# Performance work log

Measured on AMD Instinct MI355X. Metric: run time of the kernel, lower is better.

## Reference

```python
import jax, jax.numpy as jnp
import numpy as np

IN_FEAT = 512   # input_feature_size
ACT_FEAT = 512  # action_feature_size
HIDDEN = 1024   # output_feature_size
L, B = 128, 64


def setup_inputs() -> dict:
    key = jax.random.key(0)
    ks = jax.random.split(key, 4)
    scale = 1.0 / np.sqrt(HIDDEN)
    return {
        "input_feature": jax.random.normal(ks[0], (B, IN_FEAT), jnp.float32),
        "action_features_data": jax.random.normal(ks[1], (L, B, ACT_FEAT), jnp.float32),
        "hidden_state": jnp.zeros((B, HIDDEN), jnp.float32),
        "state": jnp.zeros((B, HIDDEN), jnp.float32),
        "W_ih": jax.random.normal(ks[2], (4 * HIDDEN, IN_FEAT + ACT_FEAT), jnp.float32) * scale,
        "W_hh": jax.random.normal(ks[3], (4 * HIDDEN, HIDDEN), jnp.float32) * scale,
        "b_ih": jnp.zeros((4 * HIDDEN,), jnp.float32),
        "b_hh": jnp.zeros((4 * HIDDEN,), jnp.float32),
    }


def _lstm_forward(input_feature, acts, h0, c0, W_ih, W_hh, b_ih, b_hh):
    H = h0.shape[-1]
    # Split the input weight into the static (input_feature) and per-step (action) parts.
    W_x = W_ih[:, : input_feature.shape[-1]]   # [4H, in_feat]
    W_a = W_ih[:, input_feature.shape[-1]:]    # [4H, act_feat]
    # Precompute all input-side gate preactivations in one big GEMM: [L, B, 4H]
    pre = jnp.einsum("lba,ga->lbg", acts, W_a) + (input_feature @ W_x.T + b_ih + b_hh)

    def step(carry, pre_t):
        h, c = carry
        gates = pre_t + h @ W_hh.T            # [B, 4H]
        i, f, g, o = jnp.split(gates, 4, axis=-1)  # torch LSTMCell gate order
        i = jax.nn.sigmoid(i)
        f = jax.nn.sigmoid(f)
        g = jnp.tanh(g)
        o = jax.nn.sigmoid(o)
        c1 = f * c + i * g
        h1 = o * jnp.tanh(c1)
        return (h1, c1), h1

    (h_n, c_n), hs = jax.lax.scan(step, (h0, c0), pre)
    return hs, h_n, c_n


def reference(input_feature, action_features_data, hidden_state, state,
              W_ih, W_hh, b_ih, b_hh):
    return _lstm_forward(input_feature, action_features_data, hidden_state, state,
                         W_ih, W_hh, b_ih, b_hh)
```

## Files before the change

### kernel.cpp

```cpp
#include <hip/hip_runtime.h>
#include <hip/hip_bf16.h>

typedef __bf16 bf16x8 __attribute__((ext_vector_type(8)));
typedef float f32x4 __attribute__((ext_vector_type(4)));
typedef unsigned long long ull;

#define HN_OFF 8388608u
#define CN_OFF 8454144u

__device__ __forceinline__ float bf2f(ushort u) {
  union { unsigned int i; float f; } x; x.i = ((unsigned int)u) << 16; return x.f;
}
__device__ __forceinline__ ushort f2bf(float f) {
  union { float f; unsigned int i; } x; x.f = f;
  unsigned int r = x.i + 0x7FFFu + ((x.i >> 16) & 1u);
  return (ushort)(r >> 16);
}

__global__ __launch_bounds__(256) void conv_copy(const float* __restrict__ s,
                                                 ushort* __restrict__ d, int n4) {
  int i = blockIdx.x * 256 + threadIdx.x;
  if (i < n4) {
    float4 v = reinterpret_cast<const float4*>(s)[i];
    ushort4 o; o.x = f2bf(v.x); o.y = f2bf(v.y); o.z = f2bf(v.z); o.w = f2bf(v.w);
    reinterpret_cast<ushort4*>(d)[i] = o;
  }
}

__global__ __launch_bounds__(256) void conv_h0(const float* __restrict__ h0,
                                               ushort* __restrict__ hb) {
  int t = blockIdx.x * 256 + threadIdx.x;
  int b = t >> 7, c = t & 127;
  float4 v0 = *reinterpret_cast<const float4*>(h0 + (size_t)b * 1024 + c * 8);
  float4 v1 = *reinterpret_cast<const float4*>(h0 + (size_t)b * 1024 + c * 8 + 4);
  size_t de = ((size_t)(b >> 4) * 32 + (c >> 2)) * 512 + (size_t)(c & 3) * 128 + (b & 15) * 8;
  ushort* d = hb + de;
  d[0] = f2bf(v0.x); d[1] = f2bf(v0.y); d[2] = f2bf(v0.z); d[3] = f2bf(v0.w);
  d[4] = f2bf(v1.x); d[5] = f2bf(v1.y); d[6] = f2bf(v1.z); d[7] = f2bf(v1.w);
}

__global__ __launch_bounds__(256) void conv_wa(const float* __restrict__ Wih,
                                               ushort* __restrict__ Wa) {
  int t = blockIdx.x * 256 + threadIdx.x;
  int g = t >> 7, c = t & 127;
  float4 v = *reinterpret_cast<const float4*>(Wih + (size_t)g * 1024 + 512 + c * 4);
  ushort4 o; o.x = f2bf(v.x); o.y = f2bf(v.y); o.z = f2bf(v.z); o.w = f2bf(v.w);
  *reinterpret_cast<ushort4*>(Wa + (size_t)g * 512 + c * 4) = o;
}

__global__ __launch_bounds__(256) void base_kernel(const float* __restrict__ x,
    const float* __restrict__ Wih, const float* __restrict__ bih,
    const float* __restrict__ bhh, float* __restrict__ baseT) {
  int t = blockIdx.x * 256 + threadIdx.x;
  int g = t >> 6, b = t & 63;
  const float4* xv = reinterpret_cast<const float4*>(x + (size_t)b * 512);
  const float4* wv = reinterpret_cast<const float4*>(Wih + (size_t)g * 1024);
  float s = 0.f;
  #pragma unroll 4
  for (int a = 0; a < 128; ++a) {
    float4 xa = xv[a], wa = wv[a];
    s += xa.x * wa.x + xa.y * wa.y + xa.z * wa.z + xa.w * wa.w;
  }
  baseT[t] = s + bih[g] + bhh[g];
}

__global__ __launch_bounds__(256, 1) void gemm_pre(
    const ushort* __restrict__ A,
    const ushort* __restrict__ B,
    const float* __restrict__ baseT,
    ushort* __restrict__ C) {
  __shared__ ushort At[128 * 64];
  __shared__ ushort Bt[128 * 64];
  const int tid = threadIdx.x;
  const int m0 = blockIdx.x * 128;
  const int n0 = blockIdx.y * 128;
  const int wave = tid >> 6, lane = tid & 63;
  const int wm = wave >> 1, wn = wave & 1;
  const int q = lane >> 4, lc = lane & 15;

  f32x4 acc[4][4];
  #pragma unroll
  for (int mt = 0; mt < 4; ++mt)
    #pragma unroll
    for (int nt = 0; nt < 4; ++nt)
      acc[mt][nt] = (f32x4){0.f, 0.f, 0.f, 0.f};

  for (int k0 = 0; k0 < 512; k0 += 64) {
    __syncthreads();
    for (int idx = tid; idx < 1024; idx += 256) {
      int r = idx >> 3, ch = idx & 7;
      *reinterpret_cast<uint4*>(&At[r * 64 + (ch ^ (r & 7)) * 8]) =
          *reinterpret_cast<const uint4*>(A + (size_t)(m0 + r) * 512 + k0 + ch * 8);
      *reinterpret_cast<uint4*>(&Bt[r * 64 + (ch ^ (r & 7)) * 8]) =
          *reinterpret_cast<const uint4*>(B + (size_t)(n0 + r) * 512 + k0 + ch * 8);
    }
    __syncthreads();
    #pragma unroll
    for (int kk = 0; kk < 2; ++kk) {
      bf16x8 af[4], bfr[4];
      #pragma unroll
      for (int mt = 0; mt < 4; ++mt) {
        int r = wm * 64 + mt * 16 + lc;
        af[mt] = *reinterpret_cast<const bf16x8*>(&At[r * 64 + ((kk * 4 + q) ^ (r & 7)) * 8]);
      }
      #pragma unroll
      for (int nt = 0; nt < 4; ++nt) {
        int r = wn * 64 + nt * 16 + lc;
        bfr[nt] = *reinterpret_cast<const bf16x8*>(&Bt[r * 64 + ((kk * 4 + q) ^ (r & 7)) * 8]);
      }
      #pragma unroll
      for (int mt = 0; mt < 4; ++mt)
        #pragma unroll
        for (int nt = 0; nt < 4; ++nt)
          acc[mt][nt] = __builtin_amdgcn_mfma_f32_16x16x32_bf16(af[mt], bfr[nt], acc[mt][nt], 0, 0, 0);
    }
  }
  #pragma unroll
  for (int mt = 0; mt < 4; ++mt) {
    #pragma unroll
    for (int nt = 0; nt < 4; ++nt) {
      int g = m0 + wm * 64 + mt * 16 + q * 4;
      int lb = n0 + wn * 64 + nt * 16 + lc;
      int b = lb & 63;
      #pragma unroll
      for (int i = 0; i < 4; ++i) {
        float v = acc[mt][nt][i] + baseT[(size_t)(g + i) * 64 + b];
        C[(size_t)(g + i) * 8192 + lb] = f2bf(v);
      }
    }
  }
}

#define WAITG(n) asm volatile("s_waitcnt vmcnt(" #n ")" ::: "memory"); \
                 __builtin_amdgcn_sched_barrier(0);

__global__ __launch_bounds__(256, 1) void lstm_rec(
    const ushort* __restrict__ Whh,
    const ushort* __restrict__ pre,
    const float* __restrict__ c0,
    const ushort* __restrict__ hbuf,
    ushort* __restrict__ hbw,
    float* __restrict__ out,
    int* __restrict__ flags) {
  __shared__ ushort hstage[16 * 16];
  const int tid = threadIdx.x;
  const int bid = blockIdx.x;
  const int bq = bid & 3;
  const int ug = bid >> 2;
  const int w = tid >> 6;
  const int lane = tid & 63;
  const int q = lane >> 4;
  const int lc = lane & 15;
  const int ul = w * 4 + (lc & 3);
  const int u = ug * 16 + ul;
  const int gr = u + ((lc >> 2) << 10);
  const int bbase = bq * 16 + q * 4;
  const bool cellLane = ((lc & 12) == 0);

  bf16x8 wfr[32];
  {
    const ushort* wr = Whh + (size_t)gr * 1024 + q * 8;
    #pragma unroll
    for (int kk = 0; kk < 32; ++kk)
      wfr[kk] = *reinterpret_cast<const bf16x8*>(wr + kk * 32);
  }

  float cst[4];
  #pragma unroll
  for (int i = 0; i < 4; ++i)
    cst[i] = cellLane ? c0[(size_t)(bbase + i) * 1024 + u] : 0.f;

  const unsigned va_base = ((unsigned)gr * 8192u + (unsigned)bbase) * 2u;
  const unsigned hob0 = ((unsigned)bq << 15) | ((unsigned)lane << 4);

  ushort4 pa = *reinterpret_cast<const ushort4*>(pre + (size_t)gr * 8192 + bbase);

  for (int t = 0; t < 128; ++t) {
    if (t > 0 && w == 0) {
      for (;;) {
        int f = __hip_atomic_load(&flags[(bq * 64 + lane) * 4], __ATOMIC_RELAXED,
                                  __HIP_MEMORY_SCOPE_AGENT);
        if (__all(f >= t)) break;
      }
    }
    __syncthreads();

    f32x4 acc;
    acc[0] = bf2f(pa.x); acc[1] = bf2f(pa.y); acc[2] = bf2f(pa.z); acc[3] = bf2f(pa.w);

    const int tn = (t < 127) ? t + 1 : t;
    unsigned va = va_base + (unsigned)tn * 128u;
    ushort4 npa;
    asm volatile("global_load_dwordx2 %0, %1, %2" : "=v"(npa) : "v"(va), "s"(pre));

    const unsigned hob = hob0 | ((unsigned)(t & 1) << 17);
    bf16x8 haf[32];
    #pragma unroll
    for (int kk = 0; kk < 32; ++kk) {
      unsigned voff = hob + ((unsigned)kk << 10);
      asm volatile("global_load_dwordx4 %0, %1, %2 sc0 sc1"
                   : "=v"(haf[kk]) : "v"(voff), "s"(hbuf));
    }

    #define GRP(base)                                                          \
      _Pragma("unroll")                                                        \
      for (int kk = base; kk < base + 8; ++kk)                                 \
        acc = __builtin_amdgcn_mfma_f32_16x16x32_bf16(haf[kk], wfr[kk], acc, 0, 0, 0);
    WAITG(24) GRP(0)
    WAITG(16) GRP(8)
    WAITG(8)  GRP(16)
    WAITG(0)  GRP(24)
    #undef GRP

    float fv[4], gv[4], ov[4];
    #pragma unroll
    for (int i = 0; i < 4; ++i) {
      fv[i] = __shfl_xor(acc[i], 4, 64);
      gv[i] = __shfl_xor(acc[i], 8, 64);
      ov[i] = __shfl_xor(acc[i], 12, 64);
    }
    float hv[4];
    if (cellLane) {
      #pragma unroll
      for (int i = 0; i < 4; ++i) {
        float ig = 1.f / (1.f + __expf(-acc[i]));
        float fg = 1.f / (1.f + __expf(-fv[i]));
        float gg = tanhf(gv[i]);
        float og = 1.f / (1.f + __expf(-ov[i]));
        float cn = fg * cst[i] + ig * gg;
        hv[i] = og * tanhf(cn);
        cst[i] = cn;
        hstage[(q * 4 + i) * 16 + ul] = f2bf(hv[i]);
      }
    }

    if (t == 127) {
      if (cellLane) {
        #pragma unroll
        for (int i = 0; i < 4; ++i) {
          int b = bbase + i;
          out[((size_t)t * 64 + b) * 1024 + u] = hv[i];
          out[HN_OFF + (size_t)b * 1024 + u] = hv[i];
          out[CN_OFF + (size_t)b * 1024 + u] = cst[i];
        }
      }
      break;
    }

    __syncthreads();

    if (tid < 32) {
      int bl = tid >> 1, ci = tid & 1;
      const ull* src = reinterpret_cast<const ull*>(&hstage[bl * 16 + ci * 8]);
      size_t de = ((size_t)((t + 1) & 1) << 16) + ((size_t)bq << 14) +
                  ((size_t)(ug >> 1) << 9) +
                  (size_t)(((ug * 2 + ci) & 3) * 16 + bl) * 8;
      ull* dst = reinterpret_cast<ull*>(hbw + de);
      __hip_atomic_store(dst, src[0], __ATOMIC_RELAXED, __HIP_MEMORY_SCOPE_AGENT);
      __hip_atomic_store(dst + 1, src[1], __ATOMIC_RELAXED, __HIP_MEMORY_SCOPE_AGENT);
    }
    if (w == 0) {
      asm volatile("s_waitcnt vmcnt(0)" ::: "memory");
      if (tid == 0)
        __hip_atomic_store(&flags[(bq * 64 + ug) * 4], t + 1, __ATOMIC_RELAXED,
                           __HIP_MEMORY_SCOPE_AGENT);
    }

    if (cellLane) {
      #pragma unroll
      for (int i = 0; i < 4; ++i)
        out[((size_t)t * 64 + bbase + i) * 1024 + u] = hv[i];
    }

    pa = npa;
  }
}

extern "C" void kernel_launch(void* const* d_in, const int* in_sizes, int n_in,
                              void* d_out, int out_size, void* d_ws, size_t ws_size,
                              hipStream_t stream) {
  const float* input = (const float*)d_in[0];
  const float* acts  = (const float*)d_in[1];
  const float* h0    = (const float*)d_in[2];
  const float* c0    = (const float*)d_in[3];
  const float* Wih   = (const float*)d_in[4];
  const float* Whh   = (const float*)d_in[5];
  const float* bih   = (const float*)d_in[6];
  const float* bhh   = (const float*)d_in[7];
  float* out = (float*)d_out;

  char* ws = (char*)d_ws;
  ushort* pre   = (ushort*)(ws);
  ushort* actsb = (ushort*)(ws + 67108864);
  ushort* Wab   = (ushort*)(ws + 75497472);
  ushort* Whhb  = (ushort*)(ws + 79691776);
  float*  baseT = (float*) (ws + 88080384);
  ushort* hbuf  = (ushort*)(ws + 89128960);
  int*    flags = (int*)   (ws + 89391104);

  hipMemsetAsync(flags, 0, 8192, stream);
  conv_copy<<<4096, 256, 0, stream>>>(acts, actsb, 1048576);
  conv_copy<<<4096, 256, 0, stream>>>(Whh, Whhb, 1048576);
  conv_h0<<<32, 256, 0, stream>>>(h0, hbuf);
  conv_wa<<<2048, 256, 0, stream>>>(Wih, Wab);
  base_kernel<<<1024, 256, 0, stream>>>(input, Wih, bih, bhh, baseT);
  gemm_pre<<<dim3(32, 64), 256, 0, stream>>>(Wab, actsb, baseT, pre);
  lstm_rec<<<256, 256, 0, stream>>>(Whhb, pre, c0, hbuf, hbuf, out, flags);
}
```

Baseline: 735.9 us.

## Stage hidden state through LDS cooperatively and split MFMA accumulation chain

Before, every wave loaded the full 32-chunk hidden-state fragment from global memory for each step. Now each of the 4 waves loads only 8 chunks into a shared LDS buffer, and all waves read the full K range back from LDS, cutting global traffic per block by 4x. Each wave now polls only the flags for its own slice instead of wave 0 polling all of them. The MFMA reduction is split into two independent accumulators to shorten the dependency chain. In exchange there is an extra LDS round trip, a full vmcnt(0) wait before the barrier, and the MFMAs no longer overlap with the global loads.

Result: slower. 777.4 us (+5.6%).

```diff
diff --git a/kernel.cpp b/kernel.cpp
--- a/kernel.cpp
+++ b/kernel.cpp
@@ -142,6 +142,7 @@
     ushort* __restrict__ hbw,
     float* __restrict__ out,
     int* __restrict__ flags) {
+  __shared__ ushort hl[32 * 512];
   __shared__ ushort hstage[16 * 16];
   const int tid = threadIdx.x;
   const int bid = blockIdx.x;
@@ -171,46 +172,59 @@
     cst[i] = cellLane ? c0[(size_t)(bbase + i) * 1024 + u] : 0.f;
 
   const unsigned va_base = ((unsigned)gr * 8192u + (unsigned)bbase) * 2u;
-  const unsigned hob0 = ((unsigned)bq << 15) | ((unsigned)lane << 4);
+  const unsigned hob0 = ((unsigned)bq << 15) | ((unsigned)(w * 8) << 10) |
+                        ((unsigned)lane << 4);
+  const int myflag = (bq * 64 + w * 16 + (lane & 15)) * 4;
 
   ushort4 pa = *reinterpret_cast<const ushort4*>(pre + (size_t)gr * 8192 + bbase);
 
   for (int t = 0; t < 128; ++t) {
-    if (t > 0 && w == 0) {
+    if (t > 0) {
       for (;;) {
-        int f = __hip_atomic_load(&flags[(bq * 64 + lane) * 4], __ATOMIC_RELAXED,
+        int f = __hip_atomic_load(&flags[myflag], __ATOMIC_RELAXED,
                                   __HIP_MEMORY_SCOPE_AGENT);
         if (__all(f >= t)) break;
       }
     }
+
+    const int tn = (t < 127) ? t + 1 : t;
+    ushort4 npa;
+    {
+      unsigned va = va_base + (unsigned)tn * 128u;
+      asm volatile("global_load_dwordx2 %0, %1, %2" : "=v"(npa) : "v"(va), "s"(pre));
+    }
+
+    const unsigned hob = hob0 | ((unsigned)(t & 1) << 17);
+    bf16x8 haf[8];
+    #pragma unroll
+    for (int k = 0; k < 8; ++k) {
+      unsigned voff = hob + ((unsigned)k << 10);
+      asm volatile("global_load_dwordx4 %0, %1, %2 sc0 sc1"
+                   : "=v"(haf[k]) : "v"(voff), "s"(hbuf));
+    }
+    WAITG(0)
+    #pragma unroll
+    for (int k = 0; k < 8; ++k)
+      *reinterpret_cast<bf16x8*>(&hl[(w * 8 + k) * 512 + lane * 8]) = haf[k];
     __syncthreads();
 
+    f32x4 acc_a, acc_b;
+    acc_a[0] = bf2f(pa.x); acc_a[1] = bf2f(pa.y); acc_a[2] = bf2f(pa.z); acc_a[3] = bf2f(pa.w);
+    acc_b = (f32x4){0.f, 0.f, 0.f, 0.f};
+
+    #pragma unroll
+    for (int kk = 0; kk < 16; ++kk) {
+      bf16x8 af = *reinterpret_cast<const bf16x8*>(&hl[kk * 512 + lane * 8]);
+      acc_a = __builtin_amdgcn_mfma_f32_16x16x32_bf16(af, wfr[kk], acc_a, 0, 0, 0);
+    }
+    #pragma unroll
+    for (int kk = 16; kk < 32; ++kk) {
+      bf16x8 af = *reinterpret_cast<const bf16x8*>(&hl[kk * 512 + lane * 8]);
+      acc_b = __builtin_amdgcn_mfma_f32_16x16x32_bf16(af, wfr[kk], acc_b, 0, 0, 0);
+    }
     f32x4 acc;
-    acc[0] = bf2f(pa.x); acc[1] = bf2f(pa.y); acc[2] = bf2f(pa.z); acc[3] = bf2f(pa.w);
-
-    const int tn = (t < 127) ? t + 1 : t;
-    unsigned va = va_base + (unsigned)tn * 128u;
-    ushort4 npa;
-    asm volatile("global_load_dwordx2 %0, %1, %2" : "=v"(npa) : "v"(va), "s"(pre));
-
-    const unsigned hob = hob0 | ((unsigned)(t & 1) << 17);
-    bf16x8 haf[32];
-    #pragma unroll
-    for (int kk = 0; kk < 32; ++kk) {
-      unsigned voff = hob + ((unsigned)kk << 10);
-      asm volatile("global_load_dwordx4 %0, %1, %2 sc0 sc1"
-                   : "=v"(haf[kk]) : "v"(voff), "s"(hbuf));
-    }
-
-    #define GRP(base)                                                          \
-      _Pragma("unroll")                                                        \
-      for (int kk = base; kk < base + 8; ++kk)                                 \
-        acc = __builtin_amdgcn_mfma_f32_16x16x32_bf16(haf[kk], wfr[kk], acc, 0, 0, 0);
-    WAITG(24) GRP(0)
-    WAITG(16) GRP(8)
-    WAITG(8)  GRP(16)
-    WAITG(0)  GRP(24)
-    #undef GRP
+    #pragma unroll
+    for (int i = 0; i < 4; ++i) acc[i] = acc_a[i] + acc_b[i];
 
     float fv[4], gv[4], ov[4];
     #pragma unroll
```
